# Kernel optimization log

Measured on AMD Instinct MI355X. Metric: run time of the kernel, lower is better.

The kernel has to match this reference:

```python
import jax, jax.numpy as jnp
import numpy as np

V, H, L, S = 50257, 1024, 2, 2048

def setup_inputs() -> dict:
    key = jax.random.key(0)
    ks = jax.random.split(key, 20)
    s = 0.02
    return {
        "word_input": jax.random.randint(ks[0], (1,), 0, V),
        "last_context": jax.random.normal(ks[1], (1, H), jnp.float32),
        "last_hidden": jax.random.normal(ks[2], (L, 1, H), jnp.float32),
        "encoder_outputs": jax.random.normal(ks[3], (S, 1, H), jnp.float32),
        "emb": jax.random.normal(ks[4], (V, H), jnp.float32) * s,
        "W_ih0": jax.random.normal(ks[5], (3 * H, 2 * H), jnp.float32) * s,
        "W_hh0": jax.random.normal(ks[6], (3 * H, H), jnp.float32) * s,
        "b_ih0": jax.random.normal(ks[7], (3 * H,), jnp.float32) * s,
        "b_hh0": jax.random.normal(ks[8], (3 * H,), jnp.float32) * s,
        "W_ih1": jax.random.normal(ks[9], (3 * H, H), jnp.float32) * s,
        "W_hh1": jax.random.normal(ks[10], (3 * H, H), jnp.float32) * s,
        "b_ih1": jax.random.normal(ks[11], (3 * H,), jnp.float32) * s,
        "b_hh1": jax.random.normal(ks[12], (3 * H,), jnp.float32) * s,
        "Wa": jax.random.normal(ks[13], (H, H), jnp.float32) * s,
        "ba": jax.random.normal(ks[14], (H,), jnp.float32) * s,
        "W_out": jax.random.normal(ks[15], (V, 2 * H), jnp.float32) * s,
        "b_out": jax.random.normal(ks[16], (V,), jnp.float32) * s,
    }

def gru_cell(x, h, W_ih, W_hh, b_ih, b_hh):
    # x: [1, in], h: [1, H]; PyTorch GRUCell math
    gi = x @ W_ih.T + b_ih
    gh = h @ W_hh.T + b_hh
    i_r, i_z, i_n = jnp.split(gi, 3, axis=-1)
    h_r, h_z, h_n = jnp.split(gh, 3, axis=-1)
    r = jax.nn.sigmoid(i_r + h_r)
    z = jax.nn.sigmoid(i_z + h_z)
    n = jnp.tanh(i_n + r * h_n)
    return (1.0 - z) * n + z * h

def reference(word_input, last_context, last_hidden, encoder_outputs,
              emb, W_ih0, W_hh0, b_ih0, b_hh0, W_ih1, W_hh1, b_ih1, b_hh1,
              Wa, ba, W_out, b_out):
    # embedding lookup -> [1, H]; rnn input cat(embed, context) -> [1, 2H]
    word_embedded = emb[word_input].reshape(1, -1)
    rnn_input = jnp.concatenate([word_embedded, last_context], axis=1)
    # 2-layer GRU, single timestep
    h0 = gru_cell(rnn_input, last_hidden[0], W_ih0, W_hh0, b_ih0, b_hh0)
    h1 = gru_cell(h0, last_hidden[1], W_ih1, W_hh1, b_ih1, b_hh1)
    hidden = jnp.stack([h0, h1])          # [L, 1, H]
    rnn_output = h1                       # [1, H]
    # Luong 'general' attention over encoder outputs [S, 1, H]
    enc = encoder_outputs[:, 0, :]        # [S, H]
    energy = enc @ Wa.T + ba              # [S, H]
    scores = energy @ rnn_output[0]       # [S]
    attn_w = jax.nn.softmax(scores)       # [S]
    context = (attn_w @ enc)[None, :]     # [1, H]
    logits = jnp.concatenate([rnn_output, context], axis=1) @ W_out.T + b_out
    output = jax.nn.log_softmax(logits, axis=-1)  # [1, V]
    attn_weights = attn_w[None, None, :]  # [1, 1, S]
    return output, context, hidden, attn_weights
```

## Files before the change

### kernel.cpp

```cpp
#include <hip/hip_runtime.h>
#include <hip/hip_cooperative_groups.h>

namespace cg = cooperative_groups;

namespace {

constexpr int V   = 50257;
constexpr int H   = 1024;
constexpr int SEQ = 2048;

__device__ __forceinline__ float dot4(const float4 p, const float* __restrict__ x) {
  return p.x * x[0] + p.y * x[1] + p.z * x[2] + p.w * x[3];
}

__device__ __forceinline__ float wred(float v) {
#pragma unroll
  for (int off = 32; off; off >>= 1) v += __shfl_xor(v, off, 64);
  return v;
}

__device__ __forceinline__ unsigned fenc(float x) {
  unsigned u = __float_as_uint(x);
  return u ^ ((unsigned)((int)u >> 31) | 0x80000000u);
}
__device__ __forceinline__ float fdec(unsigned k) {
  unsigned u = k ^ (((int)k >= 0) ? 0xFFFFFFFFu : 0x80000000u);
  return __uint_as_float(u);
}

__global__ __launch_bounds__(256) void k_gru0(
    const int* __restrict__ word, const float* __restrict__ emb,
    const float* __restrict__ last_context, const float* __restrict__ last_hidden0,
    const float* __restrict__ W_ih, const float* __restrict__ W_hh,
    const float* __restrict__ b_ih, const float* __restrict__ b_hh,
    float* __restrict__ h_ws, float* __restrict__ h_out)
{
  __shared__ float xs[2 * H];
  __shared__ float hs[H];
  const int tid = threadIdx.x;
  const size_t wrow = (size_t)word[0] * H;
  for (int i = tid; i < H; i += 256) {
    xs[i]     = emb[wrow + i];
    xs[H + i] = last_context[i];
    hs[i]     = last_hidden0[i];
  }
  __syncthreads();
  const int wave = tid >> 6, lane = tid & 63;
  const int j = blockIdx.x * 4 + wave;
  float acc[6];
#pragma unroll
  for (int g = 0; g < 3; ++g) {
    const float4* Wr = (const float4*)(W_ih + (size_t)(g * H + j) * (2 * H));
    float a = 0.f;
#pragma unroll
    for (int c = 0; c < 8; ++c)
      a += dot4(Wr[c * 64 + lane], &xs[c * 256 + lane * 4]);
    acc[g] = a;
  }
#pragma unroll
  for (int g = 0; g < 3; ++g) {
    const float4* Wr = (const float4*)(W_hh + (size_t)(g * H + j) * H);
    float a = 0.f;
#pragma unroll
    for (int c = 0; c < 4; ++c)
      a += dot4(Wr[c * 64 + lane], &hs[c * 256 + lane * 4]);
    acc[3 + g] = a;
  }
#pragma unroll
  for (int g = 0; g < 6; ++g) acc[g] = wred(acc[g]);
  if (lane == 0) {
    float gir = acc[0] + b_ih[j];
    float giz = acc[1] + b_ih[H + j];
    float gin = acc[2] + b_ih[2 * H + j];
    float ghr = acc[3] + b_hh[j];
    float ghz = acc[4] + b_hh[H + j];
    float ghn = acc[5] + b_hh[2 * H + j];
    float r = 1.f / (1.f + expf(-(gir + ghr)));
    float z = 1.f / (1.f + expf(-(giz + ghz)));
    float n = tanhf(gin + r * ghn);
    float h = (1.f - z) * n + z * hs[j];
    h_ws[j]  = h;
    h_out[j] = h;
  }
}

__global__ __launch_bounds__(256) void k_gru1(
    const float* __restrict__ x_ws, const float* __restrict__ last_hidden1,
    const float* __restrict__ W_ih, const float* __restrict__ W_hh,
    const float* __restrict__ b_ih, const float* __restrict__ b_hh,
    float* __restrict__ h_ws, float* __restrict__ h_out)
{
  __shared__ float xs[H];
  __shared__ float hs[H];
  const int tid = threadIdx.x;
  for (int i = tid; i < H; i += 256) {
    xs[i] = x_ws[i];
    hs[i] = last_hidden1[i];
  }
  __syncthreads();
  const int wave = tid >> 6, lane = tid & 63;
  const int j = blockIdx.x * 4 + wave;
  float acc[6];
#pragma unroll
  for (int g = 0; g < 3; ++g) {
    const float4* Wr = (const float4*)(W_ih + (size_t)(g * H + j) * H);
    float a = 0.f;
#pragma unroll
    for (int c = 0; c < 4; ++c)
      a += dot4(Wr[c * 64 + lane], &xs[c * 256 + lane * 4]);
    acc[g] = a;
  }
#pragma unroll
  for (int g = 0; g < 3; ++g) {
    const float4* Wr = (const float4*)(W_hh + (size_t)(g * H + j) * H);
    float a = 0.f;
#pragma unroll
    for (int c = 0; c < 4; ++c)
      a += dot4(Wr[c * 64 + lane], &hs[c * 256 + lane * 4]);
    acc[3 + g] = a;
  }
#pragma unroll
  for (int g = 0; g < 6; ++g) acc[g] = wred(acc[g]);
  if (lane == 0) {
    float gir = acc[0] + b_ih[j];
    float giz = acc[1] + b_ih[H + j];
    float gin = acc[2] + b_ih[2 * H + j];
    float ghr = acc[3] + b_hh[j];
    float ghz = acc[4] + b_hh[H + j];
    float ghn = acc[5] + b_hh[2 * H + j];
    float r = 1.f / (1.f + expf(-(gir + ghr)));
    float z = 1.f / (1.f + expf(-(giz + ghz)));
    float n = tanhf(gin + r * ghn);
    float h = (1.f - z) * n + z * hs[j];
    h_ws[j]  = h;
    h_out[j] = h;
  }
}

__global__ __launch_bounds__(256) void k_attn(
    const float* __restrict__ Wa, const float* __restrict__ enc,
    const float* __restrict__ h1, float* __restrict__ v,
    float* __restrict__ sc, float* __restrict__ aw,
    float* __restrict__ aw_out, float* __restrict__ ctx)
{
  cg::grid_group grid = cg::this_grid();
  __shared__ float vs[H];
  __shared__ float red[256];
  const int tid = threadIdx.x;
  const int b   = blockIdx.x;

  if (b < 64) {
    float a0 = 0.f, a1 = 0.f, a2 = 0.f, a3 = 0.f;
    for (int j = b * 16; j < b * 16 + 16; ++j) {
      float hj = h1[j];
      float4 w = ((const float4*)(Wa + (size_t)j * H))[tid];
      a0 += hj * w.x; a1 += hj * w.y; a2 += hj * w.z; a3 += hj * w.w;
    }
    atomicAdd(&v[tid * 4 + 0], a0);
    atomicAdd(&v[tid * 4 + 1], a1);
    atomicAdd(&v[tid * 4 + 2], a2);
    atomicAdd(&v[tid * 4 + 3], a3);
  }
  grid.sync();

  for (int i = tid; i < H; i += 256) vs[i] = v[i];
  __syncthreads();
  {
    const int wave = tid >> 6, lane = tid & 63;
    const int i = b * 4 + wave;
    const float4* er = (const float4*)(enc + (size_t)i * H);
    float a = 0.f;
#pragma unroll
    for (int c = 0; c < 4; ++c)
      a += dot4(er[c * 64 + lane], &vs[c * 256 + lane * 4]);
    a = wred(a);
    if (lane == 0) sc[i] = a;
  }
  grid.sync();

  if (b == 0) {
    float m = -1e30f;
    for (int k = tid; k < SEQ; k += 256) m = fmaxf(m, sc[k]);
    red[tid] = m; __syncthreads();
    for (int s = 128; s; s >>= 1) { if (tid < s) red[tid] = fmaxf(red[tid], red[tid + s]); __syncthreads(); }
    const float M = red[0]; __syncthreads();
    float sum = 0.f;
    for (int k = tid; k < SEQ; k += 256) sum += expf(sc[k] - M);
    red[tid] = sum; __syncthreads();
    for (int s = 128; s; s >>= 1) { if (tid < s) red[tid] += red[tid + s]; __syncthreads(); }
    const float inv = 1.f / red[0];
    for (int k = tid; k < SEQ; k += 256) {
      float w = expf(sc[k] - M) * inv;
      aw[k] = w;
      aw_out[k] = w;
    }
  }
  grid.sync();

  if (b < 128) {
    float a0 = 0.f, a1 = 0.f, a2 = 0.f, a3 = 0.f;
    for (int k = b * 16; k < b * 16 + 16; ++k) {
      float w = aw[k];
      float4 e = ((const float4*)(enc + (size_t)k * H))[tid];
      a0 += w * e.x; a1 += w * e.y; a2 += w * e.z; a3 += w * e.w;
    }
    atomicAdd(&ctx[tid * 4 + 0], a0);
    atomicAdd(&ctx[tid * 4 + 1], a1);
    atomicAdd(&ctx[tid * 4 + 2], a2);
    atomicAdd(&ctx[tid * 4 + 3], a3);
  }
}

__global__ __launch_bounds__(256) void k_logits(
    const float* __restrict__ h1, const float* __restrict__ ctx,
    const float* __restrict__ W_out, const float* __restrict__ b_out,
    float* __restrict__ logits, unsigned* __restrict__ maxkey,
    float* __restrict__ ctx_out)
{
  __shared__ float xs[2 * H];
  __shared__ float wmax[4];
  const int tid = threadIdx.x;
  for (int i = tid; i < H; i += 256) {
    xs[i]     = h1[i];
    xs[H + i] = ctx[i];
  }
  __syncthreads();
  if (blockIdx.x == 0) {
    for (int i = tid; i < H; i += 256) ctx_out[i] = xs[H + i];
  }
  const int wave = tid >> 6, lane = tid & 63;
  const int row = blockIdx.x * 4 + wave;
  float val = -3.0e38f;
  if (row < V) {
    const float4* Wr = (const float4*)(W_out + (size_t)row * (2 * H));
    float a = 0.f;
#pragma unroll
    for (int c = 0; c < 8; ++c)
      a += dot4(Wr[c * 64 + lane], &xs[c * 256 + lane * 4]);
    a = wred(a);
    if (lane == 0) {
      val = a + b_out[row];
      logits[row] = val;
    }
  }
  if (lane == 0) wmax[wave] = val;
  __syncthreads();
  if (tid == 0) {
    float m = fmaxf(fmaxf(wmax[0], wmax[1]), fmaxf(wmax[2], wmax[3]));
    atomicMax(maxkey, fenc(m));
  }
}

__global__ __launch_bounds__(256) void k_lse_sum(
    const float* __restrict__ logits, const unsigned* __restrict__ maxkey,
    float* __restrict__ expsum)
{
  __shared__ float red[256];
  const int tid = threadIdx.x;
  const float M = fdec(*maxkey);
  float s = 0.f;
  for (int i = blockIdx.x * 256 + tid; i < V; i += 64 * 256)
    s += expf(logits[i] - M);
  red[tid] = s; __syncthreads();
  for (int st = 128; st; st >>= 1) { if (tid < st) red[tid] += red[tid + st]; __syncthreads(); }
  if (tid == 0) atomicAdd(expsum, red[0]);
}

__global__ __launch_bounds__(256) void k_out(
    const float* __restrict__ logits, const unsigned* __restrict__ maxkey,
    const float* __restrict__ expsum, float* __restrict__ out)
{
  const int i = blockIdx.x * 256 + threadIdx.x;
  const float lse = fdec(*maxkey) + logf(*expsum);
  if (i < V) out[i] = logits[i] - lse;
}

}

extern "C" void kernel_launch(void* const* d_in, const int* in_sizes, int n_in,
                              void* d_out, int out_size, void* d_ws, size_t ws_size,
                              hipStream_t stream)
{
  const int*   word          = (const int*)d_in[0];
  const float* last_context  = (const float*)d_in[1];
  const float* last_hidden   = (const float*)d_in[2];
  const float* enc           = (const float*)d_in[3];
  const float* emb           = (const float*)d_in[4];
  const float* W_ih0         = (const float*)d_in[5];
  const float* W_hh0         = (const float*)d_in[6];
  const float* b_ih0         = (const float*)d_in[7];
  const float* b_hh0         = (const float*)d_in[8];
  const float* W_ih1         = (const float*)d_in[9];
  const float* W_hh1         = (const float*)d_in[10];
  const float* b_ih1         = (const float*)d_in[11];
  const float* b_hh1         = (const float*)d_in[12];
  const float* Wa            = (const float*)d_in[13];
  const float* W_out         = (const float*)d_in[15];
  const float* b_out         = (const float*)d_in[16];

  float* ws = (float*)d_ws;
  float*    v      = ws;
  float*    ctx    = ws + 1024;
  unsigned* maxkey = (unsigned*)(ws + 2048);
  float*    expsum = ws + 2049;
  float*    h0     = ws + 2560;
  float*    h1     = ws + 3584;
  float*    sc     = ws + 4608;
  float*    aw     = ws + 6656;
  float*    logits = ws + 8704;

  float* out     = (float*)d_out;
  float* out_ctx = out + V;
  float* out_h0  = out + V + H;
  float* out_h1  = out + V + 2 * H;
  float* out_att = out + V + 3 * H;

  hipMemsetAsync(d_ws, 0, 2304 * sizeof(float), stream);

  hipLaunchKernelGGL(k_gru0, dim3(256), dim3(256), 0, stream,
                     word, emb, last_context, last_hidden,
                     W_ih0, W_hh0, b_ih0, b_hh0, h0, out_h0);
  hipLaunchKernelGGL(k_gru1, dim3(256), dim3(256), 0, stream,
                     h0, last_hidden + H, W_ih1, W_hh1, b_ih1, b_hh1, h1, out_h1);

  {
    void* attn_args[] = {
      (void*)&Wa, (void*)&enc, (void*)&h1, (void*)&v,
      (void*)&sc, (void*)&aw, (void*)&out_att, (void*)&ctx };
    hipLaunchCooperativeKernel((void*)k_attn, dim3(512), dim3(256),
                               attn_args, 0, stream);
  }

  hipLaunchKernelGGL(k_logits, dim3((V + 3) / 4), dim3(256), 0, stream,
                     h1, ctx, W_out, b_out, logits, maxkey, out_ctx);
  hipLaunchKernelGGL(k_lse_sum, dim3(64), dim3(256), 0, stream,
                     logits, maxkey, expsum);
  hipLaunchKernelGGL(k_out, dim3((V + 255) / 256), dim3(256), 0, stream,
                     logits, maxkey, expsum, out);
}
```

Measured before the change: 954.3 us.

## Split cooperative attention kernel into three launches with redundant per-block softmax

Replaces the cooperative attention kernel and its three grid-wide syncs with three ordinary kernels: Wa^T·h1 projection, score computation, and a fused softmax+context kernel. In the last kernel every block recomputes the softmax max and sum over all 2048 scores, so the separate softmax phase and the intermediate aw buffer go away. This removes cooperative-launch and grid-barrier overhead but adds two kernel launches and redundant reduction work in each of 128 blocks.

```diff
diff --git a/kernel.cpp b/kernel.cpp
--- a/kernel.cpp
+++ b/kernel.cpp
@@ -1,7 +1,4 @@
 #include <hip/hip_runtime.h>
-#include <hip/hip_cooperative_groups.h>
-
-namespace cg = cooperative_groups;
 
 namespace {
 
@@ -137,78 +134,77 @@
   }
 }
 
-__global__ __launch_bounds__(256) void k_attn(
-    const float* __restrict__ Wa, const float* __restrict__ enc,
-    const float* __restrict__ h1, float* __restrict__ v,
-    float* __restrict__ sc, float* __restrict__ aw,
-    float* __restrict__ aw_out, float* __restrict__ ctx)
-{
-  cg::grid_group grid = cg::this_grid();
+__global__ __launch_bounds__(256) void k_wat(
+    const float* __restrict__ Wa, const float* __restrict__ h1, float* __restrict__ v)
+{
+  const int t = threadIdx.x, b = blockIdx.x;
+  float a0 = 0.f, a1 = 0.f, a2 = 0.f, a3 = 0.f;
+  for (int j = b * 16; j < b * 16 + 16; ++j) {
+    float hj = h1[j];
+    float4 w = ((const float4*)(Wa + (size_t)j * H))[t];
+    a0 += hj * w.x;
+    a1 += hj * w.y;
+    a2 += hj * w.z;
+    a3 += hj * w.w;
+  }
+  atomicAdd(&v[t * 4 + 0], a0);
+  atomicAdd(&v[t * 4 + 1], a1);
+  atomicAdd(&v[t * 4 + 2], a2);
+  atomicAdd(&v[t * 4 + 3], a3);
+}
+
+__global__ __launch_bounds__(256) void k_scores(
+    const float* __restrict__ enc, const float* __restrict__ v, float* __restrict__ sc)
+{
   __shared__ float vs[H];
+  const int tid = threadIdx.x;
+  for (int i = tid; i < H; i += 256) vs[i] = v[i];
+  __syncthreads();
+  const int wave = tid >> 6, lane = tid & 63;
+  const int i = blockIdx.x * 4 + wave;
+  const float4* er = (const float4*)(enc + (size_t)i * H);
+  float a = 0.f;
+#pragma unroll
+  for (int c = 0; c < 4; ++c)
+    a += dot4(er[c * 64 + lane], &vs[c * 256 + lane * 4]);
+  a = wred(a);
+  if (lane == 0) sc[i] = a;
+}
+
+__global__ __launch_bounds__(256) void k_ctx(
+    const float* __restrict__ enc, const float* __restrict__ sc,
+    float* __restrict__ ctx, float* __restrict__ aw_out)
+{
   __shared__ float red[256];
-  const int tid = threadIdx.x;
-  const int b   = blockIdx.x;
-
-  if (b < 64) {
-    float a0 = 0.f, a1 = 0.f, a2 = 0.f, a3 = 0.f;
-    for (int j = b * 16; j < b * 16 + 16; ++j) {
-      float hj = h1[j];
-      float4 w = ((const float4*)(Wa + (size_t)j * H))[tid];
-      a0 += hj * w.x; a1 += hj * w.y; a2 += hj * w.z; a3 += hj * w.w;
-    }
-    atomicAdd(&v[tid * 4 + 0], a0);
-    atomicAdd(&v[tid * 4 + 1], a1);
-    atomicAdd(&v[tid * 4 + 2], a2);
-    atomicAdd(&v[tid * 4 + 3], a3);
-  }
-  grid.sync();
-
-  for (int i = tid; i < H; i += 256) vs[i] = v[i];
-  __syncthreads();
-  {
-    const int wave = tid >> 6, lane = tid & 63;
-    const int i = b * 4 + wave;
-    const float4* er = (const float4*)(enc + (size_t)i * H);
-    float a = 0.f;
-#pragma unroll
-    for (int c = 0; c < 4; ++c)
-      a += dot4(er[c * 64 + lane], &vs[c * 256 + lane * 4]);
-    a = wred(a);
-    if (lane == 0) sc[i] = a;
-  }
-  grid.sync();
+  const int tid = threadIdx.x, b = blockIdx.x;
+  float m = -1e30f;
+  for (int k = tid; k < SEQ; k += 256) m = fmaxf(m, sc[k]);
+  red[tid] = m; __syncthreads();
+  for (int s = 128; s; s >>= 1) { if (tid < s) red[tid] = fmaxf(red[tid], red[tid + s]); __syncthreads(); }
+  const float M = red[0]; __syncthreads();
+  float sum = 0.f;
+  for (int k = tid; k < SEQ; k += 256) sum += expf(sc[k] - M);
+  red[tid] = sum; __syncthreads();
+  for (int s = 128; s; s >>= 1) { if (tid < s) red[tid] += red[tid + s]; __syncthreads(); }
+  const float inv = 1.f / red[0];
 
   if (b == 0) {
-    float m = -1e30f;
-    for (int k = tid; k < SEQ; k += 256) m = fmaxf(m, sc[k]);
-    red[tid] = m; __syncthreads();
-    for (int s = 128; s; s >>= 1) { if (tid < s) red[tid] = fmaxf(red[tid], red[tid + s]); __syncthreads(); }
-    const float M = red[0]; __syncthreads();
-    float sum = 0.f;
-    for (int k = tid; k < SEQ; k += 256) sum += expf(sc[k] - M);
-    red[tid] = sum; __syncthreads();
-    for (int s = 128; s; s >>= 1) { if (tid < s) red[tid] += red[tid + s]; __syncthreads(); }
-    const float inv = 1.f / red[0];
-    for (int k = tid; k < SEQ; k += 256) {
-      float w = expf(sc[k] - M) * inv;
-      aw[k] = w;
-      aw_out[k] = w;
-    }
-  }
-  grid.sync();
-
-  if (b < 128) {
-    float a0 = 0.f, a1 = 0.f, a2 = 0.f, a3 = 0.f;
-    for (int k = b * 16; k < b * 16 + 16; ++k) {
-      float w = aw[k];
-      float4 e = ((const float4*)(enc + (size_t)k * H))[tid];
-      a0 += w * e.x; a1 += w * e.y; a2 += w * e.z; a3 += w * e.w;
-    }
-    atomicAdd(&ctx[tid * 4 + 0], a0);
-    atomicAdd(&ctx[tid * 4 + 1], a1);
-    atomicAdd(&ctx[tid * 4 + 2], a2);
-    atomicAdd(&ctx[tid * 4 + 3], a3);
-  }
+    for (int k = tid; k < SEQ; k += 256) aw_out[k] = expf(sc[k] - M) * inv;
+  }
+
+  float a0 = 0.f, a1 = 0.f, a2 = 0.f, a3 = 0.f;
+  for (int k = b * 16; k < b * 16 + 16; ++k) {
+    float w = expf(sc[k] - M) * inv;
+    float4 e = ((const float4*)(enc + (size_t)k * H))[tid];
+    a0 += w * e.x;
+    a1 += w * e.y;
+    a2 += w * e.z;
+    a3 += w * e.w;
+  }
+  atomicAdd(&ctx[tid * 4 + 0], a0);
+  atomicAdd(&ctx[tid * 4 + 1], a1);
+  atomicAdd(&ctx[tid * 4 + 2], a2);
+  atomicAdd(&ctx[tid * 4 + 3], a3);
 }
 
 __global__ __launch_bounds__(256) void k_logits(
@@ -306,7 +302,6 @@
   float*    h0     = ws + 2560;
   float*    h1     = ws + 3584;
   float*    sc     = ws + 4608;
-  float*    aw     = ws + 6656;
   float*    logits = ws + 8704;
 
   float* out     = (float*)d_out;
@@ -322,15 +317,9 @@
                      W_ih0, W_hh0, b_ih0, b_hh0, h0, out_h0);
   hipLaunchKernelGGL(k_gru1, dim3(256), dim3(256), 0, stream,
                      h0, last_hidden + H, W_ih1, W_hh1, b_ih1, b_hh1, h1, out_h1);
-
-  {
-    void* attn_args[] = {
-      (void*)&Wa, (void*)&enc, (void*)&h1, (void*)&v,
-      (void*)&sc, (void*)&aw, (void*)&out_att, (void*)&ctx };
-    hipLaunchCooperativeKernel((void*)k_attn, dim3(512), dim3(256),
-                               attn_args, 0, stream);
-  }
-
+  hipLaunchKernelGGL(k_wat, dim3(64), dim3(256), 0, stream, Wa, h1, v);
+  hipLaunchKernelGGL(k_scores, dim3(SEQ / 4), dim3(256), 0, stream, enc, v, sc);
+  hipLaunchKernelGGL(k_ctx, dim3(SEQ / 16), dim3(256), 0, stream, enc, sc, ctx, out_att);
   hipLaunchKernelGGL(k_logits, dim3((V + 3) / 4), dim3(256), 0, stream,
                      h1, ctx, W_out, b_out, logits, maxkey, out_ctx);
   hipLaunchKernelGGL(k_lse_sum, dim3(64), dim3(256), 0, stream,
```

Result: faster. 774.8 us (median of 2 runs) (-18.8%).
